# Optimization experiments

Measured on AMD Instinct MI355X. Metric: run time of the kernel, lower is better.

Reference implementation:

```python
import jax, jax.numpy as jnp
import numpy as np

WS = 11      # window_size
C = 3        # channels
SIGMA = 1.5
C1 = 0.01 ** 2
C2 = 0.03 ** 2


def _gaussian_window():
    # 1D gaussian, normalized, then outer product -> [C, 1, WS, WS] depthwise kernel
    x = jnp.arange(WS, dtype=jnp.float32)
    g = jnp.exp(-((x - WS // 2) ** 2) / (2.0 * SIGMA ** 2))
    g = g / g.sum()
    w2d = jnp.outer(g, g)  # [WS, WS]
    return jnp.broadcast_to(w2d[None, None], (C, 1, WS, WS))


def _dwconv(x, w):
    # depthwise conv2d, SAME padding (pad = WS//2, odd kernel)
    pad = WS // 2
    return jax.lax.conv_general_dilated(
        x, w, window_strides=(1, 1), padding=[(pad, pad), (pad, pad)],
        dimension_numbers=("NCHW", "OIHW", "NCHW"), feature_group_count=C)


def setup_inputs() -> dict:
    key = jax.random.key(0)
    k1, k2 = jax.random.split(key)
    pred = jax.random.uniform(k1, (16, 3, 512, 512), dtype=jnp.float32)
    target = jax.random.uniform(k2, (16, 3, 512, 512), dtype=jnp.float32)
    return {"pred": pred, "target": target}


def reference(pred, target):
    w = _gaussian_window()
    mu1 = _dwconv(pred, w)
    mu2 = _dwconv(target, w)
    mu1_sq = mu1 * mu1
    mu2_sq = mu2 * mu2
    mu1_mu2 = mu1 * mu2
    sigma1_sq = _dwconv(pred * pred, w) - mu1_sq
    sigma2_sq = _dwconv(target * target, w) - mu2_sq
    sigma12 = _dwconv(pred * target, w) - mu1_mu2
    ssim_map = ((2.0 * mu1_mu2 + C1) * (2.0 * sigma12 + C2)) / (
        (mu1_sq + mu2_sq + C1) * (sigma1_sq + sigma2_sq + C2))
    return 1.0 - ssim_map.mean()
```

## Files before the change

### kernel.cpp

```cpp
#include <hip/hip_runtime.h>


#define IMG 512
#define NCHAN 48
#define TW 32
#define TH 64
#define HR (TH + 10)
#define PST 33

constexpr double RW1 = 0.8007374029168082;
constexpr double RW2 = 0.4111122905071876;
constexpr double RW3 = 0.1353352832366127;
constexpr double RW4 = 0.0285655007845504;
constexpr double RW5 = 0.0038659201394728;
constexpr double RSUM = 1.0 + 2.0 * (RW1 + RW2 + RW3 + RW4 + RW5);
constexpr float GW[11] = {
    (float)(RW5 / RSUM), (float)(RW4 / RSUM), (float)(RW3 / RSUM),
    (float)(RW2 / RSUM), (float)(RW1 / RSUM), (float)(1.0 / RSUM),
    (float)(RW1 / RSUM), (float)(RW2 / RSUM), (float)(RW3 / RSUM),
    (float)(RW4 / RSUM), (float)(RW5 / RSUM)};

__device__ __forceinline__ float2 pk_fma(float w, float2 a, float2 c) {
  return make_float2(fmaf(w, a.x, c.x), fmaf(w, a.y, c.y));
}
__device__ __forceinline__ float2 pk_mul(float2 a, float2 b) {
  return make_float2(a.x * b.x, a.y * b.y);
}

template <bool CHECKED>
__device__ __forceinline__ void hitem(const float* __restrict__ P,
                                      const float* __restrict__ T, int r0t,
                                      int c0, int j, float4 (*hs4)[PST],
                                      float (*hs1)[PST]) {
  const int g = j & 7;
  const int h = j >> 3;
  const int x0 = g * 4;
  const int gy = r0t - 5 + h;
  const int gx0 = c0 + x0 - 8;
  float2 pt[20];
  if (CHECKED) {
    const bool rowok = (gy >= 0) && (gy < IMG);
    const float* __restrict__ Prow = P + (size_t)gy * IMG;
    const float* __restrict__ Trow = T + (size_t)gy * IMG;
#pragma unroll
    for (int q = 0; q < 5; ++q) {
      const int gx = gx0 + q * 4;
      float4 vp = make_float4(0.f, 0.f, 0.f, 0.f);
      float4 vt = vp;
      if (rowok && gx >= 0 && gx < IMG) {
        vp = *(const float4*)(Prow + gx);
        vt = *(const float4*)(Trow + gx);
      }
      pt[q * 4 + 0] = make_float2(vp.x, vt.x);
      pt[q * 4 + 1] = make_float2(vp.y, vt.y);
      pt[q * 4 + 2] = make_float2(vp.z, vt.z);
      pt[q * 4 + 3] = make_float2(vp.w, vt.w);
    }
  } else {
    const float* __restrict__ Prow = P + (size_t)gy * IMG + gx0;
    const float* __restrict__ Trow = T + (size_t)gy * IMG + gx0;
#pragma unroll
    for (int q = 0; q < 5; ++q) {
      const float4 vp = *(const float4*)(Prow + q * 4);
      const float4 vt = *(const float4*)(Trow + q * 4);
      pt[q * 4 + 0] = make_float2(vp.x, vt.x);
      pt[q * 4 + 1] = make_float2(vp.y, vt.y);
      pt[q * 4 + 2] = make_float2(vp.z, vt.z);
      pt[q * 4 + 3] = make_float2(vp.w, vt.w);
    }
  }
  float2 ptsq[20];
  float ptc[20];
#pragma unroll
  for (int i = 0; i < 20; ++i) {
    ptsq[i] = pk_mul(pt[i], pt[i]);
    ptc[i] = pt[i].x * pt[i].y;
  }
#pragma unroll
  for (int o = 0; o < 4; ++o) {
    float2 smu = make_float2(0.f, 0.f);
    float2 ssq = make_float2(0.f, 0.f);
    float s12 = 0.f;
#pragma unroll
    for (int k = 0; k < 11; ++k) {
      const int i = 3 + o + k;
      const float w = GW[k];
      smu = pk_fma(w, pt[i], smu);
      ssq = pk_fma(w, ptsq[i], ssq);
      s12 = fmaf(w, ptc[i], s12);
    }
    hs4[h][x0 + o] = make_float4(smu.x, smu.y, ssq.x, ssq.y);
    hs1[h][x0 + o] = s12;
  }
}

template <bool CHECKED>
__device__ __forceinline__ void phase_b(const float* __restrict__ P,
                                        const float* __restrict__ T, int r0t,
                                        int c0, int tid, float4 (*hs4)[PST],
                                        float (*hs1)[PST]) {
  hitem<CHECKED>(P, T, r0t, c0, tid, hs4, hs1);
  hitem<CHECKED>(P, T, r0t, c0, tid + 256, hs4, hs1);
  if (tid < HR * 8 - 512) hitem<CHECKED>(P, T, r0t, c0, tid + 512, hs4, hs1);
}

__global__ __launch_bounds__(256, 3) void ssim_main(
    const float* __restrict__ pred, const float* __restrict__ tgt,
    double* __restrict__ ws) {
  __shared__ float4 hs4[HR][PST];
  __shared__ float hs1[HR][PST];
  __shared__ float wsum[4];

  const int tid = threadIdx.x;
  const int c0 = blockIdx.x * TW;
  const int r0t = blockIdx.y * TH;
  const int nc = blockIdx.z;
  const size_t base = (size_t)nc * IMG * IMG;
  const float* __restrict__ P = pred + base;
  const float* __restrict__ T = tgt + base;

  const bool interior =
      (c0 != 0) && (c0 != IMG - TW) && (r0t != 0) && (r0t != IMG - TH);
  if (interior)
    phase_b<false>(P, T, r0t, c0, tid, hs4, hs1);
  else
    phase_b<true>(P, T, r0t, c0, tid, hs4, hs1);
  __syncthreads();

  float lsum = 0.f;
  {
    const int x = tid & (TW - 1);
    const int r0 = (tid >> 5) * 8;
    float2 amu[8], asq[8];
    float a12[8];
#pragma unroll
    for (int o = 0; o < 8; ++o) {
      amu[o] = make_float2(0.f, 0.f);
      asq[o] = make_float2(0.f, 0.f);
      a12[o] = 0.f;
    }
#pragma unroll
    for (int j = 0; j < 18; ++j) {
      const float4 h4 = hs4[r0 + j][x];
      const float h1 = hs1[r0 + j][x];
      const float2 hmu = make_float2(h4.x, h4.y);
      const float2 hsq = make_float2(h4.z, h4.w);
#pragma unroll
      for (int o = 0; o < 8; ++o) {
        const int k = j - o;
        if (k >= 0 && k < 11) {
          const float w = GW[k];
          amu[o] = pk_fma(w, hmu, amu[o]);
          asq[o] = pk_fma(w, hsq, asq[o]);
          a12[o] = fmaf(w, h1, a12[o]);
        }
      }
    }
#pragma unroll
    for (int o = 0; o < 8; ++o) {
      const float s1 = amu[o].x, s2 = amu[o].y;
      const float s11 = asq[o].x, s22 = asq[o].y, s12 = a12[o];
      const float mu11 = s1 * s1;
      const float mu22 = s2 * s2;
      const float mu12 = s1 * s2;
      const float num = (2.f * mu12 + 1e-4f) * (2.f * (s12 - mu12) + 9e-4f);
      const float den =
          (mu11 + mu22 + 1e-4f) * ((s11 - mu11) + (s22 - mu22) + 9e-4f);
      lsum += num * __builtin_amdgcn_rcpf(den);
    }
  }

#pragma unroll
  for (int off = 32; off > 0; off >>= 1) lsum += __shfl_down(lsum, off, 64);
  if ((tid & 63) == 0) wsum[tid >> 6] = lsum;
  __syncthreads();
  if (tid == 0) {
    const float bsum = wsum[0] + wsum[1] + wsum[2] + wsum[3];
    unsafeAtomicAdd(&ws[nc], (double)bsum);
  }
}

__global__ void ssim_fin(const double* __restrict__ ws,
                         float* __restrict__ out) {
  const int l = threadIdx.x;
  double v = (l < NCHAN) ? ws[l] : 0.0;
#pragma unroll
  for (int off = 32; off > 0; off >>= 1) v += __shfl_down(v, off, 64);
  if (l == 0) out[0] = (float)(1.0 - v / (double)(IMG * IMG * NCHAN));
}

extern "C" void kernel_launch(void* const* d_in, const int* in_sizes, int n_in,
                              void* d_out, int out_size, void* d_ws,
                              size_t ws_size, hipStream_t stream) {
  const float* pred = (const float*)d_in[0];
  const float* tgt = (const float*)d_in[1];
  double* ws = (double*)d_ws;

  hipMemsetAsync(d_ws, 0, NCHAN * sizeof(double), stream);
  dim3 grid(IMG / TW, IMG / TH, NCHAN);
  ssim_main<<<grid, 256, 0, stream>>>(pred, tgt, ws);
  ssim_fin<<<1, 64, 0, stream>>>(ws, (float*)d_out);
}
```

Before: 181.0 us.

## Convolve sum/difference images to drop cross-product channel and shrink LDS

Replaces the five filtered quantities (p, t, p², t², pt) with four: u=p+t, v=p−t, u² and v². The means, variances and covariance are then recovered algebraically in the epilogue. This removes the separate scalar shared-memory plane and its FMAs, and frees enough LDS to raise launch bounds from 3 to 4 blocks per CU. It also batches two tiles' global loads before computing them to overlap memory latency. The risk is higher register pressure and some float cancellation in the reconstructed statistics.

After: 158.1 us. 1.14x faster.

```diff
diff --git a/kernel.cpp b/kernel.cpp
--- a/kernel.cpp
+++ b/kernel.cpp
@@ -20,24 +20,24 @@
     (float)(RW1 / RSUM), (float)(RW2 / RSUM), (float)(RW3 / RSUM),
     (float)(RW4 / RSUM), (float)(RW5 / RSUM)};
 
-__device__ __forceinline__ float2 pk_fma(float w, float2 a, float2 c) {
-  return make_float2(fmaf(w, a.x, c.x), fmaf(w, a.y, c.y));
-}
-__device__ __forceinline__ float2 pk_mul(float2 a, float2 b) {
-  return make_float2(a.x * b.x, a.y * b.y);
+__device__ __forceinline__ float2 pk_scale(float w, float2 a) {
+  return make_float2(w * a.x, w * a.y);
+}
+__device__ __forceinline__ float2 pk_add(float2 a, float2 b) {
+  return make_float2(a.x + b.x, a.y + b.y);
+}
+__device__ __forceinline__ float2 pk_fma2(float2 a, float2 b, float2 c) {
+  return make_float2(fmaf(a.x, b.x, c.x), fmaf(a.y, b.y, c.y));
 }
 
 template <bool CHECKED>
-__device__ __forceinline__ void hitem(const float* __restrict__ P,
+__device__ __forceinline__ void hload(const float* __restrict__ P,
                                       const float* __restrict__ T, int r0t,
-                                      int c0, int j, float4 (*hs4)[PST],
-                                      float (*hs1)[PST]) {
+                                      int c0, int j, float4* vp, float4* vt) {
   const int g = j & 7;
   const int h = j >> 3;
-  const int x0 = g * 4;
   const int gy = r0t - 5 + h;
-  const int gx0 = c0 + x0 - 8;
-  float2 pt[20];
+  const int gx0 = c0 + g * 4 - 8;
   if (CHECKED) {
     const bool rowok = (gy >= 0) && (gy < IMG);
     const float* __restrict__ Prow = P + (size_t)gy * IMG;
@@ -45,70 +45,72 @@
 #pragma unroll
     for (int q = 0; q < 5; ++q) {
       const int gx = gx0 + q * 4;
-      float4 vp = make_float4(0.f, 0.f, 0.f, 0.f);
-      float4 vt = vp;
+      vp[q] = make_float4(0.f, 0.f, 0.f, 0.f);
+      vt[q] = vp[q];
       if (rowok && gx >= 0 && gx < IMG) {
-        vp = *(const float4*)(Prow + gx);
-        vt = *(const float4*)(Trow + gx);
+        vp[q] = *(const float4*)(Prow + gx);
+        vt[q] = *(const float4*)(Trow + gx);
       }
-      pt[q * 4 + 0] = make_float2(vp.x, vt.x);
-      pt[q * 4 + 1] = make_float2(vp.y, vt.y);
-      pt[q * 4 + 2] = make_float2(vp.z, vt.z);
-      pt[q * 4 + 3] = make_float2(vp.w, vt.w);
     }
   } else {
     const float* __restrict__ Prow = P + (size_t)gy * IMG + gx0;
     const float* __restrict__ Trow = T + (size_t)gy * IMG + gx0;
 #pragma unroll
     for (int q = 0; q < 5; ++q) {
-      const float4 vp = *(const float4*)(Prow + q * 4);
-      const float4 vt = *(const float4*)(Trow + q * 4);
-      pt[q * 4 + 0] = make_float2(vp.x, vt.x);
-      pt[q * 4 + 1] = make_float2(vp.y, vt.y);
-      pt[q * 4 + 2] = make_float2(vp.z, vt.z);
-      pt[q * 4 + 3] = make_float2(vp.w, vt.w);
-    }
-  }
-  float2 ptsq[20];
-  float ptc[20];
-#pragma unroll
-  for (int i = 0; i < 20; ++i) {
-    ptsq[i] = pk_mul(pt[i], pt[i]);
-    ptc[i] = pt[i].x * pt[i].y;
+      vp[q] = *(const float4*)(Prow + q * 4);
+      vt[q] = *(const float4*)(Trow + q * 4);
+    }
+  }
+}
+
+__device__ __forceinline__ void hcompute(int j, const float4* vp,
+                                         const float4* vt,
+                                         float4 (*hs)[PST]) {
+  const int g = j & 7;
+  const int h = j >> 3;
+  float2 uv[20];
+#pragma unroll
+  for (int q = 0; q < 5; ++q) {
+    const float4 p4 = vp[q], t4 = vt[q];
+    uv[q * 4 + 0] = make_float2(p4.x + t4.x, p4.x - t4.x);
+    uv[q * 4 + 1] = make_float2(p4.y + t4.y, p4.y - t4.y);
+    uv[q * 4 + 2] = make_float2(p4.z + t4.z, p4.z - t4.z);
+    uv[q * 4 + 3] = make_float2(p4.w + t4.w, p4.w - t4.w);
   }
 #pragma unroll
   for (int o = 0; o < 4; ++o) {
-    float2 smu = make_float2(0.f, 0.f);
-    float2 ssq = make_float2(0.f, 0.f);
-    float s12 = 0.f;
+    float2 amu = make_float2(0.f, 0.f);
+    float2 asq = make_float2(0.f, 0.f);
 #pragma unroll
     for (int k = 0; k < 11; ++k) {
-      const int i = 3 + o + k;
-      const float w = GW[k];
-      smu = pk_fma(w, pt[i], smu);
-      ssq = pk_fma(w, ptsq[i], ssq);
-      s12 = fmaf(w, ptc[i], s12);
-    }
-    hs4[h][x0 + o] = make_float4(smu.x, smu.y, ssq.x, ssq.y);
-    hs1[h][x0 + o] = s12;
+      const float2 e = uv[3 + o + k];
+      const float2 t1 = pk_scale(GW[k], e);
+      amu = pk_add(amu, t1);
+      asq = pk_fma2(t1, e, asq);
+    }
+    hs[h][g * 4 + o] = make_float4(amu.x, amu.y, asq.x, asq.y);
   }
 }
 
 template <bool CHECKED>
 __device__ __forceinline__ void phase_b(const float* __restrict__ P,
                                         const float* __restrict__ T, int r0t,
-                                        int c0, int tid, float4 (*hs4)[PST],
-                                        float (*hs1)[PST]) {
-  hitem<CHECKED>(P, T, r0t, c0, tid, hs4, hs1);
-  hitem<CHECKED>(P, T, r0t, c0, tid + 256, hs4, hs1);
-  if (tid < HR * 8 - 512) hitem<CHECKED>(P, T, r0t, c0, tid + 512, hs4, hs1);
-}
-
-__global__ __launch_bounds__(256, 3) void ssim_main(
+                                        int c0, int tid, float4 (*hs)[PST]) {
+  float4 ap[5], at[5], bp[5], bt[5];
+  hload<CHECKED>(P, T, r0t, c0, tid, ap, at);
+  hload<CHECKED>(P, T, r0t, c0, tid + 256, bp, bt);
+  hcompute(tid, ap, at, hs);
+  hcompute(tid + 256, bp, bt, hs);
+  if (tid < HR * 8 - 512) {
+    hload<CHECKED>(P, T, r0t, c0, tid + 512, ap, at);
+    hcompute(tid + 512, ap, at, hs);
+  }
+}
+
+__global__ __launch_bounds__(256, 4) void ssim_main(
     const float* __restrict__ pred, const float* __restrict__ tgt,
     double* __restrict__ ws) {
-  __shared__ float4 hs4[HR][PST];
-  __shared__ float hs1[HR][PST];
+  __shared__ float4 hs[HR][PST];
   __shared__ float wsum[4];
 
   const int tid = threadIdx.x;
@@ -122,9 +124,9 @@
   const bool interior =
       (c0 != 0) && (c0 != IMG - TW) && (r0t != 0) && (r0t != IMG - TH);
   if (interior)
-    phase_b<false>(P, T, r0t, c0, tid, hs4, hs1);
+    phase_b<false>(P, T, r0t, c0, tid, hs);
   else
-    phase_b<true>(P, T, r0t, c0, tid, hs4, hs1);
+    phase_b<true>(P, T, r0t, c0, tid, hs);
   __syncthreads();
 
   float lsum = 0.f;
@@ -132,17 +134,14 @@
     const int x = tid & (TW - 1);
     const int r0 = (tid >> 5) * 8;
     float2 amu[8], asq[8];
-    float a12[8];
 #pragma unroll
     for (int o = 0; o < 8; ++o) {
       amu[o] = make_float2(0.f, 0.f);
       asq[o] = make_float2(0.f, 0.f);
-      a12[o] = 0.f;
     }
 #pragma unroll
     for (int j = 0; j < 18; ++j) {
-      const float4 h4 = hs4[r0 + j][x];
-      const float h1 = hs1[r0 + j][x];
+      const float4 h4 = hs[r0 + j][x];
       const float2 hmu = make_float2(h4.x, h4.y);
       const float2 hsq = make_float2(h4.z, h4.w);
 #pragma unroll
@@ -150,22 +149,22 @@
         const int k = j - o;
         if (k >= 0 && k < 11) {
           const float w = GW[k];
-          amu[o] = pk_fma(w, hmu, amu[o]);
-          asq[o] = pk_fma(w, hsq, asq[o]);
-          a12[o] = fmaf(w, h1, a12[o]);
+          amu[o] = pk_fma2(make_float2(w, w), hmu, amu[o]);
+          asq[o] = pk_fma2(make_float2(w, w), hsq, asq[o]);
         }
       }
     }
 #pragma unroll
     for (int o = 0; o < 8; ++o) {
-      const float s1 = amu[o].x, s2 = amu[o].y;
-      const float s11 = asq[o].x, s22 = asq[o].y, s12 = a12[o];
-      const float mu11 = s1 * s1;
-      const float mu22 = s2 * s2;
-      const float mu12 = s1 * s2;
+      const float cu = amu[o].x, cv = amu[o].y;
+      const float cu2 = asq[o].x, cv2 = asq[o].y;
+      const float cusq = cu * cu, cvsq = cv * cv;
+      const float mu12 = 0.25f * (cusq - cvsq);
+      const float musq = 0.5f * (cusq + cvsq);
+      const float s12 = 0.25f * (cu2 - cv2);
+      const float ssq = 0.5f * (cu2 + cv2);
       const float num = (2.f * mu12 + 1e-4f) * (2.f * (s12 - mu12) + 9e-4f);
-      const float den =
-          (mu11 + mu22 + 1e-4f) * ((s11 - mu11) + (s22 - mu22) + 9e-4f);
+      const float den = (musq + 1e-4f) * (ssq - musq + 9e-4f);
       lsum += num * __builtin_amdgcn_rcpf(den);
     }
   }
```
